# Kernel optimization log

Measured on AMD Instinct MI355X. Metric: run time of the kernel, lower is better.

Reference implementation:

```python
import math
import jax, jax.numpy as jnp
import numpy as np

# ---- static config (mirrors init_kwargs) ----
NLAT_I, NLON_I = 240, 480      # input equiangular grid (incl. both poles)
NLAT_O, NLON_O = 361, 720      # output equiangular grid (incl. both poles)
CI, CO = 32, 32
NR, NPHI = 3, 3                # kernel_shape
K = (NR - 1) * NPHI + 1        # anisotropic piecewise-linear DISCO basis size = 7
LMAX = 120
CUTOFF = (NR + 0.25) * math.pi / LMAX     # _compute_cutoff_radius
DLAT_O = math.pi / (NLAT_O - 1)
WOFF = int(math.ceil(CUTOFF / DLAT_O))    # half lat-window (=10); geodesic dist >= |dtheta| so window is exact
WLAT = 2 * WOFF + 1
TWO_PI = 2.0 * math.pi


def _bilinear_upsample(x):
    # ResampleS2(mode='bilinear'): x [B,C,NLAT_I,NLON_I] -> [B,C,NLAT_O,NLON_O]
    # equiangular colatitudes theta_j = pi*j/(nlat-1); periodic longitude.
    pos_t = jnp.linspace(0.0, math.pi, NLAT_O) / (math.pi / (NLAT_I - 1))
    i0 = jnp.clip(jnp.floor(pos_t).astype(jnp.int32), 0, NLAT_I - 1)
    i1 = jnp.minimum(i0 + 1, NLAT_I - 1)
    wt = (pos_t - i0).astype(x.dtype)
    xl = (1.0 - wt)[:, None] * x[:, :, i0, :] + wt[:, None] * x[:, :, i1, :]
    pos_p = (jnp.arange(NLON_O) * (TWO_PI / NLON_O)) / (TWO_PI / NLON_I)
    j0f = jnp.floor(pos_p)
    j0 = j0f.astype(jnp.int32) % NLON_I
    j1 = (j0 + 1) % NLON_I
    wp = (pos_p - j0f).astype(x.dtype)
    return (1.0 - wp) * xl[..., j0] + wp * xl[..., j1]


def _build_psi():
    # DISCO filter tensor psi[k, t_out, dlat, dlon] with quadrature merged in,
    # exploiting longitude translation invariance (computed at lon_out = 0).
    theta = jnp.linspace(0.0, math.pi, NLAT_O)
    t_idx = jnp.arange(NLAT_O)
    d_idx = jnp.arange(WLAT) - WOFF
    lat_in = t_idx[:, None] + d_idx[None, :]             # [T,W]
    valid = (lat_in >= 0) & (lat_in < NLAT_O)
    lat_in_c = jnp.clip(lat_in, 0, NLAT_O - 1)
    alpha = -theta[:, None, None]                         # [T,1,1]
    gamma = theta[lat_in_c][:, :, None]                   # [T,W,1]
    beta = (TWO_PI / NLON_O) * jnp.arange(NLON_O)[None, None, :]
    # rotate input point into frame where the output point is at the north pole
    z = jnp.cos(alpha) * jnp.cos(gamma) - jnp.cos(beta) * jnp.sin(alpha) * jnp.sin(gamma)
    xx = jnp.cos(alpha) * jnp.cos(beta) * jnp.sin(gamma) + jnp.sin(alpha) * jnp.cos(gamma)
    yy = jnp.sin(beta) * jnp.sin(gamma)
    r = jnp.arccos(jnp.clip(z, -1.0, 1.0))                # geodesic distance [T,W,P]
    phi = jnp.arctan2(yy, xx) % TWO_PI                    # local azimuth
    dr = CUTOFF / NR
    dph = TWO_PI / NPHI
    vals = [jnp.maximum(0.0, 1.0 - r / dr)]               # isotropic center hat
    for k in range(1, K):
        ir = (k - 1) // NPHI + 1
        ip = (k - 1) % NPHI
        rad = jnp.maximum(0.0, 1.0 - jnp.abs(r - ir * dr) / dr)
        dd = jnp.abs(phi - ip * dph)
        dd = jnp.minimum(dd, TWO_PI - dd)
        az = jnp.maximum(0.0, 1.0 - dd / dph)
        vals.append(rad * az)
    psi = jnp.stack(vals, 0)                              # [K,T,W,P]
    psi = psi * (r <= CUTOFF) * valid[None, :, :, None]
    # merge quadrature weights of the input grid (sin(theta) dtheta dphi)
    q = jnp.sin(theta) * (math.pi / (NLAT_O - 1)) * (TWO_PI / NLON_O)
    psi = psi * q[lat_in_c][None, :, :, None]
    # nodal L1 normalization per basis function and output node
    scale = jnp.sum(psi, axis=(2, 3), keepdims=True)
    psi = psi / jnp.maximum(scale, 1e-8)
    return psi.astype(jnp.float32), lat_in_c


def _disco_conv(xu, weight, psi, lat_in_c):
    # xu [B,Ci,T,P]; weight [Co,Ci,K]; psi [K,T,W,P]
    h = jnp.einsum('oik,bitp->boktp', weight, xu)         # fold channel mixing first
    Hh = jnp.fft.rfft(h, axis=-1)                         # [B,Co,K,T,F]
    Ph = jnp.conj(jnp.fft.rfft(psi, axis=-1))             # [K,T,W,F]
    yh = jnp.zeros(Hh.shape[:2] + (NLAT_O, Hh.shape[-1]), dtype=Hh.dtype)
    for d in range(WLAT):                                 # small fixed halo loop
        Hd = Hh[:, :, :, lat_in_c[:, d], :]               # [B,Co,K,T,F]
        yh = yh + jnp.einsum('boktf,ktf->botf', Hd, Ph[:, :, d, :])
    return jnp.fft.irfft(yh, n=NLON_O, axis=-1)           # circular correlation over lon


def setup_inputs() -> dict:
    key = jax.random.key(0)
    k1, k2 = jax.random.split(key)
    x = jax.random.normal(k1, (1, CI, NLAT_I, NLON_I), dtype=jnp.float32)
    weight = jax.random.normal(k2, (CO, CI, K), dtype=jnp.float32) * 0.05
    return {'x': x, 'weight': weight}


def reference(x, weight):
    psi, lat_in_c = _build_psi()
    xu = _bilinear_upsample(x.astype(jnp.float32))        # forced fp32 region
    y = _disco_conv(xu, weight.astype(jnp.float32), psi, lat_in_c)
    return y.astype(x.dtype)
```

## Files before the change

kernel.cpp:

```cpp
#include <hip/hip_runtime.h>
#include <hip/hip_bf16.h>
#include <math.h>

#define NLAT_I 240
#define NLON_I 480
#define NLAT_O 361
#define NLON_O 720
#define CI_N 32
#define CO_N 32
#define K_N 7
#define WOFF 10
#define WLAT 21

#define PI_F 3.14159265358979323846f
#define TWOPI_F 6.28318530717958647692f
#define DLAT_V (PI_F / 360.0f)
#define DPHI_V (TWOPI_F / 720.0f)
#define CUTOFF_V (3.25f * PI_F / 120.0f)
#define DR_V (CUTOFF_V / 3.0f)
#define IDR_V (1.0f / DR_V)
#define DPH_V (TWOPI_F / 3.0f)
#define IDPH_V (1.0f / DPH_V)
#define QF_V (DLAT_V * DPHI_V)

#define PAD_T 64
#define CT 64
#define NBLK 256
#define NC45 45
#define NE 7581

typedef __attribute__((ext_vector_type(8))) short short8v;
typedef __attribute__((ext_vector_type(4))) short short4v;
typedef __attribute__((ext_vector_type(16))) float f32x16;

__device__ __forceinline__ unsigned short f2bf(float f) {
  __hip_bfloat16 h = __float2bfloat16(f);
  union { __hip_bfloat16 b; unsigned short s; } u; u.b = h; return u.s;
}

typedef __attribute__((address_space(1))) const unsigned int ga_u32_t;
typedef __attribute__((address_space(3))) unsigned int ls_u32_t;
__device__ __forceinline__ void dma16(const unsigned short* g, unsigned short* l) {
  __builtin_amdgcn_global_load_lds((ga_u32_t*)(const void*)g,
                                   (ls_u32_t*)(void*)l, 16, 0, 0);
}

__device__ __forceinline__ void psi_eval(float ct, float st, float cg, float sg,
                                         float q, float bang, float v[7]) {
  float sb, cb;
  sincosf(bang, &sb, &cb);
  float dx = sg * cb - st;
  float dy = sg * sb;
  float dz = cg - ct;
  float c2 = dx * dx + dy * dy + dz * dz;
  float r = 2.0f * asinf(fminf(1.0f, 0.5f * sqrtf(c2)));
  if (r <= CUTOFF_V) {
    float xx = ct * cb * sg - st * cg;
    float yy = sb * sg;
    float phi = atan2f(yy, xx);
    if (phi < 0.0f) phi += TWOPI_F;
    v[0] = fmaxf(0.0f, 1.0f - r * IDR_V) * q;
#pragma unroll
    for (int k = 1; k < 7; ++k) {
      const float irdr = (float)(1 + (k - 1) / 3) * DR_V;
      const float ipph = (float)((k - 1) % 3) * DPH_V;
      float rad = fmaxf(0.0f, 1.0f - fabsf(r - irdr) * IDR_V);
      float dd = fabsf(phi - ipph);
      dd = fminf(dd, TWOPI_F - dd);
      float az = fmaxf(0.0f, 1.0f - dd * IDPH_V);
      v[k] = rad * az * q;
    }
  } else {
#pragma unroll
    for (int k = 0; k < 7; ++k) v[k] = 0.0f;
  }
}

__device__ __forceinline__ int windowB(int t, int d) {
  int tp = t + d - WOFF;
  if (tp < 0 || tp > NLAT_O - 1) return -1;
  float th = (float)t * DLAT_V, ga = (float)tp * DLAT_V;
  float st = sinf(th), ct = cosf(th), sg = sinf(ga), cg = cosf(ga);
  float den = st * sg;
  float num = cosf(CUTOFF_V) - ct * cg;
  if (den < 1e-9f) return (fabsf(th - ga) <= CUTOFF_V) ? 360 : -1;
  if (num >= den) return -1;
  if (num <= -den) return 360;
  int B = (int)ceilf(acosf(num / den) * (1.0f / DPHI_V)) + 1;
  return B > 360 ? 360 : B;
}

__device__ __forceinline__ int nsupOf(int B) { return (B >= 360) ? 720 : 2 * B + 1; }
__device__ __forceinline__ int widthOf(int B) {
  return (B < 0) ? 0 : ((nsupOf(B) + 129) & ~1);
}

__global__ void prep_kernel(const float* __restrict__ w, unsigned short* __restrict__ w2,
                            int* __restrict__ offsF, int* __restrict__ offsT,
                            int* __restrict__ wtab, float* __restrict__ sums,
                            int* __restrict__ counter, int* __restrict__ gB,
                            int* __restrict__ gUc) {
  const int tid = threadIdx.x;
  __shared__ int temp[256];
  if (tid < 8) counter[tid] = 0;
  for (int idx = tid; idx < 361 * 7; idx += 256) sums[idx] = 0.0f;
  for (int idx = tid; idx < 14 * 32 * 16; idx += 256) {
    int kk = idx & 15; int o = (idx >> 4) & 31; int c16 = idx >> 9;
    int ci = c16 * 16 + kk; int i = ci & 31; int k = ci >> 5;
    w2[idx] = f2bf(w[(o * 32 + i) * 7 + k]);
  }
  for (int e = tid; e < NE; e += 256) {
    int t = e / 21, d = e % 21;
    int B = windowB(t, d);
    gB[e] = B;
    offsF[e] = (B >= 0) ? nsupOf(B) * 7 : 0;
    offsT[e] = 14 * widthOf(B);
  }
  __syncthreads();
  for (int t = tid; t < 361; t += 256) {
    int run = 0;
    for (int d = 0; d < WLAT; ++d) {
      gUc[t * 22 + d] = run;
      int B = gB[t * 21 + d];
      int np = (B >= 0) ? ((31 + B) >> 4) + ((B + 15) >> 4) + 1 : 0;
      run += np;
    }
    gUc[t * 22 + 21] = run;
    wtab[t] = run;
  }
  __syncthreads();
#pragma unroll 1
  for (int pass = 0; pass < 2; ++pass) {
    int* a = pass ? offsT : offsF;
    int s = tid * 30, e = s + 30; if (e > NE) e = NE; if (s > NE) s = NE;
    int sum = 0;
    for (int i = s; i < e; ++i) sum += a[i];
    temp[tid] = sum;
    __syncthreads();
    if (tid == 0) {
      int run = 0;
      for (int i = 0; i < 256; ++i) { int v = temp[i]; temp[i] = run; run += v; }
      a[NE] = run;
    }
    __syncthreads();
    int run = temp[tid];
    for (int i = s; i < e; ++i) { int v = a[i]; a[i] = run; run += v; }
    __syncthreads();
  }
}

__global__ void upsample_kernel(const float* __restrict__ x,
                                unsigned short* __restrict__ XT) {
  int idx = blockIdx.x * 256 + threadIdx.x;
  if (idx >= NLAT_O * NC45 * 512) return;
  int kk = idx & 15;
  int i = (idx >> 4) & 31;
  int c = (idx >> 9) % NC45;
  int t = idx / (NC45 * 512);
  int p = c * 16 + kk;

  double post = (double)t * (239.0 / 360.0);
  int i0 = (int)floor(post);
  if (i0 < 0) i0 = 0;
  if (i0 > NLAT_I - 1) i0 = NLAT_I - 1;
  int i1 = i0 + 1; if (i1 > NLAT_I - 1) i1 = NLAT_I - 1;
  float wt = (float)(post - (double)i0);

  double posp = (double)p * (2.0 / 3.0);
  double j0f = floor(posp);
  int j0 = ((int)j0f) % NLON_I;
  int j1 = (j0 + 1) % NLON_I;
  float wp = (float)(posp - j0f);

  const float* xi = x + (size_t)i * (NLAT_I * NLON_I);
  float a = xi[i0 * NLON_I + j0];
  float b = xi[i0 * NLON_I + j1];
  float cc = xi[i1 * NLON_I + j0];
  float d = xi[i1 * NLON_I + j1];
  float l0 = (1.0f - wt) * a + wt * cc;
  float l1 = (1.0f - wt) * b + wt * d;
  XT[idx] = f2bf((1.0f - wp) * l0 + wp * l1);
}

__global__ void psi_raw_kernel(const int* __restrict__ offsF,
                               float* __restrict__ PSIF,
                               float* __restrict__ sums) {
  int t = blockIdx.x, d = blockIdx.y;
  int B = windowB(t, d);
  if (B < 0) return;
  int nsup = nsupOf(B);
  int bLo = (B >= 360) ? -360 : -B;
  int offF = offsF[t * 21 + d];
  int tp = t + d - WOFF;
  float th = (float)t * DLAT_V, ga = (float)tp * DLAT_V;
  float st, ct, sg, cg;
  sincosf(th, &st, &ct);
  sincosf(ga, &sg, &cg);
  float q = sg * QF_V;
  float acc[7];
#pragma unroll
  for (int k = 0; k < 7; ++k) acc[k] = 0.0f;
  for (int ix = threadIdx.x; ix < nsup; ix += 256) {
    float v[7];
    psi_eval(ct, st, cg, sg, q, (float)(bLo + ix) * DPHI_V, v);
#pragma unroll
    for (int k = 0; k < 7; ++k) { PSIF[offF + k * nsup + ix] = v[k]; acc[k] += v[k]; }
  }
#pragma unroll
  for (int k = 0; k < 7; ++k) {
    float a = acc[k];
    for (int off = 32; off > 0; off >>= 1) a += __shfl_down(a, off, 64);
    acc[k] = a;
  }
  __shared__ float red[4][7];
  int wid = threadIdx.x >> 6;
  if ((threadIdx.x & 63) == 0) {
#pragma unroll
    for (int k = 0; k < 7; ++k) red[wid][k] = acc[k];
  }
  __syncthreads();
  if (threadIdx.x == 0) {
#pragma unroll
    for (int k = 0; k < 7; ++k)
      atomicAdd(&sums[t * 7 + k], red[0][k] + red[1][k] + red[2][k] + red[3][k]);
  }
}

__global__ void psi_toep_kernel(const int* __restrict__ offsF,
                                const int* __restrict__ offsT,
                                const float* __restrict__ PSIF,
                                const float* __restrict__ sums,
                                unsigned short* __restrict__ PSIT) {
  int t = blockIdx.x, d = blockIdx.y;
  int B = windowB(t, d);
  if (B < 0) return;
  int nsup = nsupOf(B);
  int width = widthOf(B);
  int offF = offsF[t * 21 + d];
  int offT = offsT[t * 21 + d];
  float rc[7];
#pragma unroll
  for (int k = 0; k < 7; ++k) rc[k] = 1.0f / fmaxf(sums[t * 7 + k], 1e-8f);
  for (int ix = threadIdx.x; ix <= width; ix += 256) {
    int isup = ix - PAD_T;
    unsigned short vv[7];
    if (isup >= 0 && isup < nsup) {
#pragma unroll
      for (int k = 0; k < 7; ++k)
        vv[k] = f2bf(PSIF[offF + k * nsup + isup] * rc[k]);
    } else {
#pragma unroll
      for (int k = 0; k < 7; ++k) vv[k] = 0;
    }
    if (ix < width) {
#pragma unroll
      for (int k = 0; k < 7; ++k) PSIT[offT + (2 * k) * width + ix] = vv[k];
    }
    if (ix >= 1) {
#pragma unroll
      for (int k = 0; k < 7; ++k) PSIT[offT + (2 * k + 1) * width + ix - 1] = vv[k];
    }
  }
}


#define VMW16 asm volatile("s_waitcnt vmcnt(16)" ::: "memory");
#define BARR  __builtin_amdgcn_s_barrier();

#define STAGEU(IDX) {                                                       \
    int ix_ = (IDX); if (ix_ > nUm1) ix_ = nUm1;                            \
    int mx_ = __builtin_amdgcn_readlane(mxL, ix_);                          \
    int my_ = __builtin_amdgcn_readlane(myL, ix_);                          \
    int wdt_ = my_ & 4095;                                                  \
    int dd_ = (my_ >> 12) & 31;                                             \
    int cc_ = ((my_ >> 17) & 63) - 32;                                      \
    int sl_ = ix_ & 7;                                                      \
    int jb_ = mx_ + lconst;                                                 \
    const unsigned short* bs_ = PSIT + jb_ + ((jb_ & 1) ? (wdt_ - 1) : 0);  \
    unsigned short* bd_ = Bring + sl_ * 3584;                               \
    int ks_ = 2 * wdt_;                                                     \
    dma16(bs_ + r0B * ks_, bd_ + (r0B << 9));                               \
    dma16(bs_ + r1B * ks_, bd_ + (r1B << 9));                               \
    int v45_ = pw16 + cc_;                                                  \
    if (v45_ < 0) v45_ += NC45;                                             \
    if (v45_ >= NC45) v45_ -= NC45;                                         \
    int v45b_ = v45_ + 2; if (v45b_ >= NC45) v45b_ -= NC45;                 \
    int tpd_ = t + dd_ - WOFF;                                              \
    unsigned short* ad_ = Aring + (((wv << 3) + sl_) << 10);                \
    dma16(XT + (((size_t)(tpd_ * NC45 + v45_)) << 9) + laneA, ad_);         \
    dma16(XT + (((size_t)(tpd_ * NC45 + v45b_)) << 9) + laneA, ad_ + 512); }

#define READF(S, IDX) {                                                     \
    int sl_ = (IDX) & 7;                                                    \
    const unsigned short* bb_ = Bring + sl_ * 3584 + (lane << 3);           \
    B##S##0 = *(const short8v*)(bb_);                                       \
    B##S##1 = *(const short8v*)(bb_ + 512);                                 \
    B##S##2 = *(const short8v*)(bb_ + 1024);                                \
    B##S##3 = *(const short8v*)(bb_ + 1536);                                \
    B##S##4 = *(const short8v*)(bb_ + 2048);                                \
    B##S##5 = *(const short8v*)(bb_ + 2560);                                \
    B##S##6 = *(const short8v*)(bb_ + 3072);                                \
    const unsigned short* aa_ = Aring + (((wv << 3) + sl_) << 10) + (lane << 3); \
    A##S##a = *(const short8v*)(aa_);                                       \
    A##S##b = *(const short8v*)(aa_ + 512); }

#define MFMA14(S) {                                                         \
    accA0 = __builtin_amdgcn_mfma_f32_32x32x16_bf16(A##S##a, B##S##0, accA0, 0, 0, 0); \
    accB0 = __builtin_amdgcn_mfma_f32_32x32x16_bf16(A##S##b, B##S##0, accB0, 0, 0, 0); \
    accA1 = __builtin_amdgcn_mfma_f32_32x32x16_bf16(A##S##a, B##S##1, accA1, 0, 0, 0); \
    accB1 = __builtin_amdgcn_mfma_f32_32x32x16_bf16(A##S##b, B##S##1, accB1, 0, 0, 0); \
    accA2 = __builtin_amdgcn_mfma_f32_32x32x16_bf16(A##S##a, B##S##2, accA2, 0, 0, 0); \
    accB2 = __builtin_amdgcn_mfma_f32_32x32x16_bf16(A##S##b, B##S##2, accB2, 0, 0, 0); \
    accA3 = __builtin_amdgcn_mfma_f32_32x32x16_bf16(A##S##a, B##S##3, accA3, 0, 0, 0); \
    accB3 = __builtin_amdgcn_mfma_f32_32x32x16_bf16(A##S##b, B##S##3, accB3, 0, 0, 0); \
    accA4 = __builtin_amdgcn_mfma_f32_32x32x16_bf16(A##S##a, B##S##4, accA4, 0, 0, 0); \
    accB4 = __builtin_amdgcn_mfma_f32_32x32x16_bf16(A##S##b, B##S##4, accB4, 0, 0, 0); \
    accA5 = __builtin_amdgcn_mfma_f32_32x32x16_bf16(A##S##a, B##S##5, accA5, 0, 0, 0); \
    accB5 = __builtin_amdgcn_mfma_f32_32x32x16_bf16(A##S##b, B##S##5, accB5, 0, 0, 0); \
    accA6 = __builtin_amdgcn_mfma_f32_32x32x16_bf16(A##S##a, B##S##6, accA6, 0, 0, 0); \
    accB6 = __builtin_amdgcn_mfma_f32_32x32x16_bf16(A##S##b, B##S##6, accB6, 0, 0, 0); }

#define DUMP2(ACC, KK, HB) {                                              \
    short4v q_;                                                           \
    q_[0]=(short)f2bf(ACC[8*(HB)+0]); q_[1]=(short)f2bf(ACC[8*(HB)+1]);   \
    q_[2]=(short)f2bf(ACC[8*(HB)+2]); q_[3]=(short)f2bf(ACC[8*(HB)+3]);   \
    *(short4v*)(b2 + ((KK) << 9) + b0_) = q_;                             \
    q_[0]=(short)f2bf(ACC[8*(HB)+4]); q_[1]=(short)f2bf(ACC[8*(HB)+5]);   \
    q_[2]=(short)f2bf(ACC[8*(HB)+6]); q_[3]=(short)f2bf(ACC[8*(HB)+7]);   \
    *(short4v*)(b2 + ((KK) << 9) + b0_ + 8) = q_; }

#define GEMM2PT(AC0, AC1, AC2, AC3, AC4, AC5, AC6, PTILE) {               \
    f32x16 Dy;                                                            \
    _Pragma("unroll") for (int z = 0; z < 16; ++z) Dy[z] = 0.0f;          \
    DUMP2(AC0, 0, 0) DUMP2(AC1, 1, 0) DUMP2(AC2, 2, 0) DUMP2(AC3, 3, 0)  \
    DUMP2(AC4, 4, 0) DUMP2(AC5, 5, 0) DUMP2(AC6, 6, 0)                    \
    _Pragma("unroll") for (int k2 = 0; k2 < 7; ++k2) {                    \
      short8v A2 = *(const short8v*)(w2g + (((2 * k2 + 0) * 32 + nn) << 4) + g8); \
      short8v B2f = *(const short8v*)(b2 + (k2 << 9) + (nn << 4) + g8);   \
      Dy = __builtin_amdgcn_mfma_f32_32x32x16_bf16(A2, B2f, Dy, 0, 0, 0); \
    }                                                                     \
    DUMP2(AC0, 0, 1) DUMP2(AC1, 1, 1) DUMP2(AC2, 2, 1) DUMP2(AC3, 3, 1)  \
    DUMP2(AC4, 4, 1) DUMP2(AC5, 5, 1) DUMP2(AC6, 6, 1)                    \
    _Pragma("unroll") for (int k2 = 0; k2 < 7; ++k2) {                    \
      short8v A2 = *(const short8v*)(w2g + (((2 * k2 + 1) * 32 + nn) << 4) + g8); \
      short8v B2f = *(const short8v*)(b2 + (k2 << 9) + (nn << 4) + g8);   \
      Dy = __builtin_amdgcn_mfma_f32_32x32x16_bf16(A2, B2f, Dy, 0, 0, 0); \
    }                                                                     \
    const int p_ = (PTILE) * 32 + nn;                                     \
    if (p_ < NLON_O) {                                                    \
      _Pragma("unroll") for (int rr = 0; rr < 16; ++rr) {                 \
        int o = (rr & 3) + 8 * (rr >> 2) + 4 * g;                         \
        atomicAdd(&y[((size_t)o * NLAT_O + t) * NLON_O + p_], Dy[rr]);    \
      }                                                                   \
    } }

__global__ __launch_bounds__(256, 1) void disco_kernel(
    const unsigned short* __restrict__ XT, const unsigned short* __restrict__ PSIT,
    const unsigned short* __restrict__ w2g, const int* __restrict__ offsT,
    const int* __restrict__ wtab, const int* __restrict__ gB,
    const int* __restrict__ gUc, float* __restrict__ y,
    int* __restrict__ counter) {
  const int tid = threadIdx.x;
  __shared__ __align__(16) unsigned short Bring[8 * 3584];
  __shared__ __align__(16) unsigned short Aring[32 * 1024];
  __shared__ __align__(16) unsigned short b2all[4 * 3584];
  __shared__ int Sbuf[362];
  __shared__ int sB[WLAT], sUc[WLAT + 1], sOff[WLAT], sW[WLAT];
  __shared__ int curItem, sSv;

  for (int j = tid; j < 361; j += 256) {
    int t = (j & 1) ? 360 - (j >> 1) : (j >> 1);
    Sbuf[j] = 3 * ((wtab[t] + CT - 1) / CT);
  }
  __syncthreads();
  if (tid == 0) {
    int run = 0;
    for (int j = 0; j < 361; ++j) { int v = Sbuf[j]; Sbuf[j] = run; run += v; }
    Sbuf[361] = run;
    sSv = 0;
  }
  __syncthreads();
  const int NTOT = Sbuf[361];
  const int xcd = blockIdx.x & 7;

  const int lane = tid & 63, wv = tid >> 6, nn = lane & 31, g = lane >> 5;
  const int g8 = g * 8;
  const int laneA = nn * 16 + g8;
  const int lconst = g8 - nn;
  const int r0B = (wv < 3) ? 2 * wv : 6;
  const int r1B = (wv < 3) ? 2 * wv + 1 : 6;

  while (true) {
    if (tid == 0) {
      int mm = NTOT;
      int s2 = sSv;
      while (s2 < 8) {
        int cx = (xcd + s2) & 7;
        int b0 = (NTOT * cx) >> 3;
        int b1 = (NTOT * (cx + 1)) >> 3;
        int off = atomicAdd(&counter[cx], 1);
        if (b0 + off < b1) { mm = b0 + off; break; }
        ++s2;
      }
      sSv = s2;
      curItem = mm;
    }
    __syncthreads();
    const int m = curItem;
    if (m >= NTOT) break;

    int lo = 0, hi = 360;
    while (lo < hi) {
      int mid = (lo + hi + 1) >> 1;
      if (Sbuf[mid] <= m) lo = mid; else hi = mid - 1;
    }
    const int j = lo;
    const int r = m - Sbuf[j];
    const int t = (j & 1) ? 360 - (j >> 1) : (j >> 1);
    const int pgpair = r % 3;
    const int part = r / 3;

    if (tid < WLAT) {
      int B = gB[t * 21 + tid];
      sB[tid] = B;
      sOff[tid] = offsT[t * 21 + tid];
      sW[tid] = widthOf(B);
    }
    if (tid < WLAT + 1) sUc[tid] = gUc[t * 22 + tid];
    __syncthreads();

    const int Wt = sUc[WLAT];
    int g0 = part * CT, g1 = g0 + CT;
    if (g1 > Wt) g1 = Wt;
    const int nU = g1 - g0;
    const int nUm1 = nU - 1;

    const int ptileA = pgpair * 8 + 2 * wv;
    const int pw16 = ptileA * 2;

    int mxL, myL;
    {
      int uu_ = lane; if (uu_ > nUm1) uu_ = nUm1;
      int ug_ = g0 + uu_;
      int dd = 0;
      while (dd < 20 && sUc[dd + 1] <= ug_) ++dd;
      int Bv = sB[dd];
      int bLo_ = (Bv >= 360) ? -360 : -Bv;
      int cc_ = -((Bv + 15) >> 4) + (ug_ - sUc[dd]);
      mxL = sOff[dd] + cc_ * 16 - bLo_ + PAD_T;
      myL = sW[dd] | (dd << 12) | ((cc_ + 32) << 17);
    }

    f32x16 accA0, accA1, accA2, accA3, accA4, accA5, accA6;
    f32x16 accB0, accB1, accB2, accB3, accB4, accB5, accB6;
#pragma unroll
    for (int z = 0; z < 16; ++z) {
      accA0[z]=0; accA1[z]=0; accA2[z]=0; accA3[z]=0; accA4[z]=0; accA5[z]=0; accA6[z]=0;
      accB0[z]=0; accB1[z]=0; accB2[z]=0; accB3[z]=0; accB4[z]=0; accB5[z]=0; accB6[z]=0;
    }

    short8v AXa, AXb, BX0, BX1, BX2, BX3, BX4, BX5, BX6;
    short8v AYa, AYb, BY0, BY1, BY2, BY3, BY4, BY5, BY6;

    STAGEU(0) STAGEU(1) STAGEU(2) STAGEU(3) STAGEU(4)
    VMW16 BARR
    READF(X, 0)

    int u = 0;
    while (true) {
      STAGEU(u + 5)
      VMW16 BARR
      int nx = u + 1; bool h1 = (nx < nU); if (!h1) nx = u;
      READF(Y, nx)
      MFMA14(X)
      if (!h1) break;
      STAGEU(u + 6)
      VMW16 BARR
      int nx2 = u + 2; bool h2 = (nx2 < nU); if (!h2) nx2 = nx;
      READF(X, nx2)
      MFMA14(Y)
      if (!h2) break;
      u += 2;
    }

    unsigned short* b2 = b2all + wv * 3584;
    const int b0_ = nn * 16 + 4 * g;
    GEMM2PT(accA0, accA1, accA2, accA3, accA4, accA5, accA6, ptileA)
    GEMM2PT(accB0, accB1, accB2, accB3, accB4, accB5, accB6, ptileA + 1)
  }
}

extern "C" void kernel_launch(void* const* d_in, const int* in_sizes, int n_in,
                              void* d_out, int out_size, void* d_ws, size_t ws_size,
                              hipStream_t stream) {
  (void)in_sizes; (void)n_in; (void)out_size; (void)ws_size;
  const float* x = (const float*)d_in[0];
  const float* w = (const float*)d_in[1];
  float* y = (float*)d_out;

  unsigned short* XT = (unsigned short*)d_ws;
  float* PSIF = (float*)(XT + (size_t)NLAT_O * NC45 * 512);
  unsigned short* PSIT = (unsigned short*)(PSIF + 6000000);
  unsigned short* w2 = PSIT + 26000000;
  float* sums = (float*)(w2 + 7168);
  int* offsF = (int*)(sums + NLAT_O * K_N);
  int* offsT = offsF + NE + 1;
  int* wtab = offsT + NE + 1;
  int* counter = wtab + 361;
  int* gB = counter + 8;
  int* gUc = gB + NE;

  hipMemsetAsync(y, 0, (size_t)CO_N * NLAT_O * NLON_O * sizeof(float), stream);

  prep_kernel<<<1, 256, 0, stream>>>(w, w2, offsF, offsT, wtab, sums, counter, gB, gUc);
  int n_up = NLAT_O * NC45 * 512;
  upsample_kernel<<<(n_up + 255) / 256, 256, 0, stream>>>(x, XT);
  psi_raw_kernel<<<dim3(NLAT_O, WLAT), 256, 0, stream>>>(offsF, PSIF, sums);
  psi_toep_kernel<<<dim3(NLAT_O, WLAT), 256, 0, stream>>>(offsF, offsT, PSIF, sums, PSIT);
  disco_kernel<<<NBLK, 256, 0, stream>>>(XT, PSIT, w2, offsT, wtab, gB, gUc, y, counter);
}
```

Before: 480.6 us.

## Load A fragments directly from global into registers, drop LDS A ring

The A operand (input activations) is no longer DMA'd into a shared-memory ring. Each wave now loads it straight from global memory into registers two steps ahead of use. The B (psi) prefetch depth drops from five stages to three, with matching vmcnt waits. This removes LDS traffic and footprint for A and shortens the pipeline, at the cost of exposing global-load latency in registers and increasing register pressure.

```diff
diff --git a/kernel.cpp b/kernel.cpp
--- a/kernel.cpp
+++ b/kernel.cpp
@@ -264,34 +264,39 @@
 }
 
 
-#define VMW16 asm volatile("s_waitcnt vmcnt(16)" ::: "memory");
+#define VMW6 asm volatile("s_waitcnt vmcnt(6)" ::: "memory");
+#define VMW4 asm volatile("s_waitcnt vmcnt(4)" ::: "memory");
 #define BARR  __builtin_amdgcn_s_barrier();
 
-#define STAGEU(IDX) {                                                       \
+#define STAGEB(IDX) {                                                       \
     int ix_ = (IDX); if (ix_ > nUm1) ix_ = nUm1;                            \
     int mx_ = __builtin_amdgcn_readlane(mxL, ix_);                          \
     int my_ = __builtin_amdgcn_readlane(myL, ix_);                          \
     int wdt_ = my_ & 4095;                                                  \
-    int dd_ = (my_ >> 12) & 31;                                             \
-    int cc_ = ((my_ >> 17) & 63) - 32;                                      \
     int sl_ = ix_ & 7;                                                      \
     int jb_ = mx_ + lconst;                                                 \
     const unsigned short* bs_ = PSIT + jb_ + ((jb_ & 1) ? (wdt_ - 1) : 0);  \
     unsigned short* bd_ = Bring + sl_ * 3584;                               \
     int ks_ = 2 * wdt_;                                                     \
     dma16(bs_ + r0B * ks_, bd_ + (r0B << 9));                               \
-    dma16(bs_ + r1B * ks_, bd_ + (r1B << 9));                               \
+    dma16(bs_ + r1B * ks_, bd_ + (r1B << 9)); }
+
+#define ALOAD(S, IDX) {                                                     \
+    int ix_ = (IDX); if (ix_ > nUm1) ix_ = nUm1;                            \
+    int my_ = __builtin_amdgcn_readlane(myL, ix_);                          \
+    int dd_ = (my_ >> 12) & 31;                                             \
+    int cc_ = ((my_ >> 17) & 63) - 32;                                      \
     int v45_ = pw16 + cc_;                                                  \
     if (v45_ < 0) v45_ += NC45;                                             \
     if (v45_ >= NC45) v45_ -= NC45;                                         \
     int v45b_ = v45_ + 2; if (v45b_ >= NC45) v45b_ -= NC45;                 \
-    int tpd_ = t + dd_ - WOFF;                                              \
-    unsigned short* ad_ = Aring + (((wv << 3) + sl_) << 10);                \
-    dma16(XT + (((size_t)(tpd_ * NC45 + v45_)) << 9) + laneA, ad_);         \
-    dma16(XT + (((size_t)(tpd_ * NC45 + v45b_)) << 9) + laneA, ad_ + 512); }
-
-#define READF(S, IDX) {                                                     \
-    int sl_ = (IDX) & 7;                                                    \
+    const unsigned short* ab_ = XT + (((size_t)((t + dd_ - WOFF) * NC45)) << 9) + laneA; \
+    A##S##a = *(const short8v*)(ab_ + ((size_t)v45_ << 9));                 \
+    A##S##b = *(const short8v*)(ab_ + ((size_t)v45b_ << 9)); }
+
+#define READB(S, IDX) {                                                     \
+    int ix_ = (IDX); if (ix_ > nUm1) ix_ = nUm1;                            \
+    int sl_ = ix_ & 7;                                                      \
     const unsigned short* bb_ = Bring + sl_ * 3584 + (lane << 3);           \
     B##S##0 = *(const short8v*)(bb_);                                       \
     B##S##1 = *(const short8v*)(bb_ + 512);                                 \
@@ -299,10 +304,7 @@
     B##S##3 = *(const short8v*)(bb_ + 1536);                                \
     B##S##4 = *(const short8v*)(bb_ + 2048);                                \
     B##S##5 = *(const short8v*)(bb_ + 2560);                                \
-    B##S##6 = *(const short8v*)(bb_ + 3072);                                \
-    const unsigned short* aa_ = Aring + (((wv << 3) + sl_) << 10) + (lane << 3); \
-    A##S##a = *(const short8v*)(aa_);                                       \
-    A##S##b = *(const short8v*)(aa_ + 512); }
+    B##S##6 = *(const short8v*)(bb_ + 3072); }
 
 #define MFMA14(S) {                                                         \
     accA0 = __builtin_amdgcn_mfma_f32_32x32x16_bf16(A##S##a, B##S##0, accA0, 0, 0, 0); \
@@ -319,6 +321,13 @@
     accB5 = __builtin_amdgcn_mfma_f32_32x32x16_bf16(A##S##b, B##S##5, accB5, 0, 0, 0); \
     accA6 = __builtin_amdgcn_mfma_f32_32x32x16_bf16(A##S##a, B##S##6, accA6, 0, 0, 0); \
     accB6 = __builtin_amdgcn_mfma_f32_32x32x16_bf16(A##S##b, B##S##6, accB6, 0, 0, 0); }
+
+#define PHASE(SCUR, SNXT, UCUR)                                             \
+    STAGEB((UCUR) + 3)                                                      \
+    VMW6 BARR                                                               \
+    READB(SNXT, (UCUR) + 1)                                                 \
+    MFMA14(SCUR)                                                            \
+    ALOAD(SCUR, (UCUR) + 2)
 
 #define DUMP2(ACC, KK, HB) {                                              \
     short4v q_;                                                           \
@@ -362,7 +371,6 @@
     int* __restrict__ counter) {
   const int tid = threadIdx.x;
   __shared__ __align__(16) unsigned short Bring[8 * 3584];
-  __shared__ __align__(16) unsigned short Aring[32 * 1024];
   __shared__ __align__(16) unsigned short b2all[4 * 3584];
   __shared__ int Sbuf[362];
   __shared__ int sB[WLAT], sUc[WLAT + 1], sOff[WLAT], sW[WLAT];
@@ -462,24 +470,17 @@
     short8v AXa, AXb, BX0, BX1, BX2, BX3, BX4, BX5, BX6;
     short8v AYa, AYb, BY0, BY1, BY2, BY3, BY4, BY5, BY6;
 
-    STAGEU(0) STAGEU(1) STAGEU(2) STAGEU(3) STAGEU(4)
-    VMW16 BARR
-    READF(X, 0)
+    ALOAD(X, 0) ALOAD(Y, 1)
+    STAGEB(0) STAGEB(1) STAGEB(2)
+    VMW4 BARR
+    READB(X, 0)
 
     int u = 0;
     while (true) {
-      STAGEU(u + 5)
-      VMW16 BARR
-      int nx = u + 1; bool h1 = (nx < nU); if (!h1) nx = u;
-      READF(Y, nx)
-      MFMA14(X)
-      if (!h1) break;
-      STAGEU(u + 6)
-      VMW16 BARR
-      int nx2 = u + 2; bool h2 = (nx2 < nU); if (!h2) nx2 = nx;
-      READF(X, nx2)
-      MFMA14(Y)
-      if (!h2) break;
+      PHASE(X, Y, u)
+      if (u + 1 >= nU) break;
+      PHASE(Y, X, u + 1)
+      if (u + 2 >= nU) break;
       u += 2;
     }
 
```

Result: slower. 641.3 us (+33.4%).

## Double column chunk size, stage two slots per barrier, vectorize epilogue stores

Applied to the files above, without the earlier changes.

Raises the per-block column chunk from 64 to 128 and splits the per-lane metadata over two registers so each block covers more work. The main loop now issues two stage loads per barrier and drops the second barrier each iteration, halving sync points, with a tighter vmcnt wait. The epilogue writes 8 bf16 values in one store, and the weight packing is permuted to match the new layout. Risks include fewer blocks per row, less load balance, and a shallower prefetch lead per barrier.

```diff
diff --git a/kernel.cpp b/kernel.cpp
--- a/kernel.cpp
+++ b/kernel.cpp
@@ -24,7 +24,7 @@
 #define QF_V (DLAT_V * DPHI_V)
 
 #define PAD_T 64
-#define CT 64
+#define CT 128
 #define NBLK 256
 #define NC45 45
 #define NE 7581
@@ -106,7 +106,8 @@
   for (int idx = tid; idx < 361 * 7; idx += 256) sums[idx] = 0.0f;
   for (int idx = tid; idx < 14 * 32 * 16; idx += 256) {
     int kk = idx & 15; int o = (idx >> 4) & 31; int c16 = idx >> 9;
-    int ci = c16 * 16 + kk; int i = ci & 31; int k = ci >> 5;
+    int il = 4 * (kk >> 3) + (kk & 3) + 8 * ((kk >> 2) & 1);
+    int i = (c16 & 1) * 16 + il; int k = c16 >> 1;
     w2[idx] = f2bf(w[(o * 32 + i) * 7 + k]);
   }
   for (int e = tid; e < NE; e += 256) {
@@ -264,13 +265,19 @@
 }
 
 
-#define VMW16 asm volatile("s_waitcnt vmcnt(16)" ::: "memory");
+#define VMW8 asm volatile("s_waitcnt vmcnt(8)" ::: "memory");
 #define BARR  __builtin_amdgcn_s_barrier();
+
+#define GETMETA(IX) \
+    int mx_, my_; \
+    if ((IX) & 64) { mx_ = __builtin_amdgcn_readlane(mxL1, (IX) & 63); \
+                     my_ = __builtin_amdgcn_readlane(myL1, (IX) & 63); } \
+    else           { mx_ = __builtin_amdgcn_readlane(mxL0, (IX) & 63); \
+                     my_ = __builtin_amdgcn_readlane(myL0, (IX) & 63); }
 
 #define STAGEU(IDX) {                                                       \
     int ix_ = (IDX); if (ix_ > nUm1) ix_ = nUm1;                            \
-    int mx_ = __builtin_amdgcn_readlane(mxL, ix_);                          \
-    int my_ = __builtin_amdgcn_readlane(myL, ix_);                          \
+    GETMETA(ix_)                                                            \
     int wdt_ = my_ & 4095;                                                  \
     int dd_ = (my_ >> 12) & 31;                                             \
     int cc_ = ((my_ >> 17) & 63) - 32;                                      \
@@ -321,13 +328,12 @@
     accB6 = __builtin_amdgcn_mfma_f32_32x32x16_bf16(A##S##b, B##S##6, accB6, 0, 0, 0); }
 
 #define DUMP2(ACC, KK, HB) {                                              \
-    short4v q_;                                                           \
+    short8v q_;                                                           \
     q_[0]=(short)f2bf(ACC[8*(HB)+0]); q_[1]=(short)f2bf(ACC[8*(HB)+1]);   \
     q_[2]=(short)f2bf(ACC[8*(HB)+2]); q_[3]=(short)f2bf(ACC[8*(HB)+3]);   \
-    *(short4v*)(b2 + ((KK) << 9) + b0_) = q_;                             \
-    q_[0]=(short)f2bf(ACC[8*(HB)+4]); q_[1]=(short)f2bf(ACC[8*(HB)+5]);   \
-    q_[2]=(short)f2bf(ACC[8*(HB)+6]); q_[3]=(short)f2bf(ACC[8*(HB)+7]);   \
-    *(short4v*)(b2 + ((KK) << 9) + b0_ + 8) = q_; }
+    q_[4]=(short)f2bf(ACC[8*(HB)+4]); q_[5]=(short)f2bf(ACC[8*(HB)+5]);   \
+    q_[6]=(short)f2bf(ACC[8*(HB)+6]); q_[7]=(short)f2bf(ACC[8*(HB)+7]);   \
+    *(short8v*)(b2 + ((KK) << 9) + b0_) = q_; }
 
 #define GEMM2PT(AC0, AC1, AC2, AC3, AC4, AC5, AC6, PTILE) {               \
     f32x16 Dy;                                                            \
@@ -438,17 +444,19 @@
     const int ptileA = pgpair * 8 + 2 * wv;
     const int pw16 = ptileA * 2;
 
-    int mxL, myL;
-    {
-      int uu_ = lane; if (uu_ > nUm1) uu_ = nUm1;
+    int mxL0, myL0, mxL1, myL1;
+#pragma unroll
+    for (int hfu = 0; hfu < 2; ++hfu) {
+      int uu_ = lane + hfu * 64; if (uu_ > nUm1) uu_ = nUm1;
       int ug_ = g0 + uu_;
       int dd = 0;
       while (dd < 20 && sUc[dd + 1] <= ug_) ++dd;
       int Bv = sB[dd];
       int bLo_ = (Bv >= 360) ? -360 : -Bv;
       int cc_ = -((Bv + 15) >> 4) + (ug_ - sUc[dd]);
-      mxL = sOff[dd] + cc_ * 16 - bLo_ + PAD_T;
-      myL = sW[dd] | (dd << 12) | ((cc_ + 32) << 17);
+      int mxv = sOff[dd] + cc_ * 16 - bLo_ + PAD_T;
+      int myv = sW[dd] | (dd << 12) | ((cc_ + 32) << 17);
+      if (hfu == 0) { mxL0 = mxv; myL0 = myv; } else { mxL1 = mxv; myL1 = myv; }
     }
 
     f32x16 accA0, accA1, accA2, accA3, accA4, accA5, accA6;
@@ -462,20 +470,18 @@
     short8v AXa, AXb, BX0, BX1, BX2, BX3, BX4, BX5, BX6;
     short8v AYa, AYb, BY0, BY1, BY2, BY3, BY4, BY5, BY6;
 
-    STAGEU(0) STAGEU(1) STAGEU(2) STAGEU(3) STAGEU(4)
-    VMW16 BARR
+    STAGEU(0) STAGEU(1) STAGEU(2) STAGEU(3)
+    VMW8 BARR
     READF(X, 0)
 
     int u = 0;
     while (true) {
-      STAGEU(u + 5)
-      VMW16 BARR
+      STAGEU(u + 4) STAGEU(u + 5)
+      VMW8 BARR
       int nx = u + 1; bool h1 = (nx < nU); if (!h1) nx = u;
       READF(Y, nx)
       MFMA14(X)
       if (!h1) break;
-      STAGEU(u + 6)
-      VMW16 BARR
       int nx2 = u + 2; bool h2 = (nx2 < nU); if (!h2) nx2 = nx;
       READF(X, nx2)
       MFMA14(Y)
@@ -484,7 +490,7 @@
     }
 
     unsigned short* b2 = b2all + wv * 3584;
-    const int b0_ = nn * 16 + 4 * g;
+    const int b0_ = nn * 16 + g8;
     GEMM2PT(accA0, accA1, accA2, accA3, accA4, accA5, accA6, ptileA)
     GEMM2PT(accB0, accB1, accB2, accB3, accB4, accB5, accB6, ptileA + 1)
   }
```

New measurement: 478.0 us. About the same (-0.5%).
